# Kernel tuning notes

Hardware: AMD Instinct MI355X
Metric: run time of the kernel (lower is better)

The kernel has to match this reference:

```python
import jax, jax.numpy as jnp
import numpy as np

B, T, IN, H, OUT = 1024, 512, 16, 64, 8


def setup_inputs() -> dict:
    key = jax.random.key(0)
    ks = jax.random.split(key, 7)
    s = 1.0 / np.sqrt(H)
    return {
        "x": jax.random.normal(ks[0], (B, T, IN), dtype=jnp.float32),
        "W_ih": jax.random.normal(ks[1], (4 * H, IN), dtype=jnp.float32) * s,
        "W_hh": jax.random.normal(ks[2], (4 * H, H), dtype=jnp.float32) * s,
        "b_ih": jax.random.normal(ks[3], (4 * H,), dtype=jnp.float32) * s,
        "b_hh": jax.random.normal(ks[4], (4 * H,), dtype=jnp.float32) * s,
        "W_fc": jax.random.normal(ks[5], (OUT, H), dtype=jnp.float32) * s,
        "b_fc": jax.random.normal(ks[6], (OUT,), dtype=jnp.float32) * s,
    }


def reference(x, W_ih, W_hh, b_ih, b_hh, W_fc, b_fc):
    Bq, Tq, _ = x.shape
    Hq = W_hh.shape[1]
    # Precompute input contribution for all timesteps: [T, B, 4H]
    xw = jnp.einsum("bti,gi->tbg", x, W_ih) + b_ih + b_hh

    def step(carry, xw_t):
        h, c = carry
        gates = xw_t + h @ W_hh.T  # [B, 4H]
        i, f, g, o = jnp.split(gates, 4, axis=-1)  # PyTorch gate order i,f,g,o
        i = jax.nn.sigmoid(i)
        f = jax.nn.sigmoid(f)
        g = jnp.tanh(g)
        o = jax.nn.sigmoid(o)
        c = f * c + i * g
        h = o * jnp.tanh(c)
        return (h, c), None

    h0 = jnp.zeros((Bq, Hq), dtype=x.dtype)
    c0 = jnp.zeros((Bq, Hq), dtype=x.dtype)
    (h_last, _), _ = jax.lax.scan(step, (h0, c0), xw)

    # fc on last timestep only, then sigmoid -> [B, 1, OUT]
    out = jax.nn.sigmoid(h_last @ W_fc.T + b_fc)
    return out[:, None, :]
```

## Files before the change

kernel.cpp:

```cpp
#include <hip/hip_runtime.h>
#include <math.h>


#define LSTM_T 512
#define LSTM_IN 16
#define LSTM_H 64
#define LSTM_OUT 8
#define BT 2
#define HSTRIDE 80

#define L2E   1.44269504088896340736f
#define L2E2  2.88539008177792681472f

typedef _Float16 half8  __attribute__((ext_vector_type(8)));
typedef float    floatx4 __attribute__((ext_vector_type(4)));

static __device__ __forceinline__ float fast_rcp(float x) { return __builtin_amdgcn_rcpf(x); }
static __device__ __forceinline__ float fast_exp2(float x) { return __builtin_amdgcn_exp2f(x); }
static __device__ __forceinline__ float sigm2(float p) { return fast_rcp(1.0f + fast_exp2(-p)); }
static __device__ __forceinline__ void pin4(int4& v) {
    asm volatile("" : "+v"(v.x), "+v"(v.y), "+v"(v.z), "+v"(v.w));
}
static __device__ __forceinline__ void pinf4(float4& v) {
    asm volatile("" : "+v"(v.x), "+v"(v.y), "+v"(v.z), "+v"(v.w));
}
static __device__ __forceinline__ void lite_barrier() {
    asm volatile("s_waitcnt lgkmcnt(0)\n\ts_barrier" ::: "memory");
}
static __device__ __forceinline__ unsigned pk2h(float a, float b) {
    return __builtin_bit_cast(unsigned, __builtin_amdgcn_cvt_pkrtz(a, b));
}
static __device__ __forceinline__ half8 to_h8(float4 a, float4 b) {
    uint4 u = make_uint4(pk2h(a.x, a.y), pk2h(a.z, a.w), pk2h(b.x, b.y), pk2h(b.z, b.w));
    return __builtin_bit_cast(half8, u);
}
static __device__ __forceinline__ int4 cvt8h(float4 a, float4 b) {
    return __builtin_bit_cast(int4, to_h8(a, b));
}
static __device__ __forceinline__ float4 ld4(const float* p) {
    return *reinterpret_cast<const float4*>(p);
}
static __device__ __forceinline__ float4 scl4(float4 v, float s) {
    return make_float4(s * v.x, s * v.y, s * v.z, s * v.w);
}
static __device__ __forceinline__ float sel4(floatx4 v, bool r0, bool r1) {
    float lo = r0 ? v[1] : v[0];
    float hi = r0 ? v[3] : v[2];
    return r1 ? hi : lo;
}
static __device__ __forceinline__ float dpp8(float v) {
    int r = __builtin_amdgcn_update_dpp(0, __builtin_bit_cast(int, v),
                                        0x128, 0xF, 0xF, false);
    return __builtin_bit_cast(float, r);
}

__global__ __launch_bounds__(256, 2)
void lstm_mfma_kernel(const float* __restrict__ x,
                      const float* __restrict__ W_ih,
                      const float* __restrict__ W_hh,
                      const float* __restrict__ b_ih,
                      const float* __restrict__ b_hh,
                      const float* __restrict__ W_fc,
                      const float* __restrict__ b_fc,
                      float* __restrict__ out) {
    const int tid   = threadIdx.x;
    const int lane  = tid & 63;
    const int w     = tid >> 6;
    const int q     = lane >> 4;
    const int m     = lane & 15;
    const int b     = m & 1;
    const int rho   = (m >> 1) & 3;
    const bool r0   = (rho & 1) != 0;
    const bool r1   = (rho & 2) != 0;
    const bool h1   = (m & 8) != 0;
    const int jmine = 16 * w + 4 * q + rho;
    const int bbase = blockIdx.x * BT;

    const float a1 = h1 ? 1.0f : 0.0f;
    const float b1 = h1 ? -2.0f : 1.0f;

    __shared__ __align__(128) _Float16 hbuf[2][BT][HSTRIDE];
    __shared__ __align__(16)  float    hfin[BT][LSTM_H];

    int4 Ah[4][2], Ax[4];
    float4 bias4[4];
    #pragma unroll
    for (int tt = 0; tt < 4; ++tt) {
        const float sc = (tt == 2) ? L2E2 : -L2E;
        const int gt = tt * 64 + 16 * w + m;
        #pragma unroll
        for (int c = 0; c < 2; ++c) {
            const float* s = W_hh + gt * LSTM_H + 32 * c + 8 * q;
            Ah[tt][c] = cvt8h(scl4(ld4(s), sc), scl4(ld4(s + 4), sc));
            pin4(Ah[tt][c]);
        }
        float4 xa = make_float4(0.f, 0.f, 0.f, 0.f), xb = xa;
        if (q < 2) {
            const float* s = W_ih + gt * LSTM_IN + 8 * q;
            xa = ld4(s); xb = ld4(s + 4);
        }
        Ax[tt] = cvt8h(scl4(xa, sc), scl4(xb, sc));
        pin4(Ax[tt]);
        const int gb = tt * 64 + 16 * w + 4 * q;
        float4 bi = ld4(b_ih + gb), bh = ld4(b_hh + gb);
        bias4[tt] = make_float4(sc * (bi.x + bh.x), sc * (bi.y + bh.y),
                                sc * (bi.z + bh.z), sc * (bi.w + bh.w));
        pinf4(bias4[tt]);
    }

    if (tid < 80) {
        reinterpret_cast<int*>(&hbuf[0][0][0])[tid] = 0;
    }

    const float* xp = x + (size_t)(bbase + b) * LSTM_T * LSTM_IN + 8 * q;
    float4 xA0 = make_float4(0.f, 0.f, 0.f, 0.f), xA1 = xA0;
    float4 xB0 = xA0, xB1 = xA0;
    if (q < 2) {
        xA0 = ld4(xp);              xA1 = ld4(xp + 4);
        xB0 = ld4(xp + LSTM_IN);    xB1 = ld4(xp + LSTM_IN + 4);
    }

    floatx4 accX[4];
    {
        half8 xf = to_h8(xA0, xA1);
        #pragma unroll
        for (int tt = 0; tt < 4; ++tt)
            accX[tt] = __builtin_amdgcn_mfma_f32_16x16x32_f16(
                __builtin_bit_cast(half8, Ax[tt]), xf,
                __builtin_bit_cast(floatx4, bias4[tt]), 0, 0, 0);
    }
    if (q < 2) {
        xA0 = ld4(xp + 2 * LSTM_IN);
        xA1 = ld4(xp + 2 * LSTM_IN + 4);
    }
    __syncthreads();

    float cs = 0.0f, hreg = 0.0f;

#define STEP(T_, X0, X1)                                                        \
    {                                                                           \
        const _Float16* cur = &hbuf[(T_) & 1][0][0];                            \
        _Float16*       nxt = &hbuf[((T_) + 1) & 1][0][0];                      \
               \
        half8 bh0 = *reinterpret_cast<const half8*>(cur + b * HSTRIDE + 8 * q); \
        half8 bh1 = *reinterpret_cast<const half8*>(cur + b * HSTRIDE + 32 + 8 * q); \
                \
        floatx4 accf, accg, acci, acco;                                         \
        accf = __builtin_amdgcn_mfma_f32_16x16x32_f16(                          \
            __builtin_bit_cast(half8, Ah[1][0]), bh0, accX[1], 0, 0, 0);        \
        accg = __builtin_amdgcn_mfma_f32_16x16x32_f16(                          \
            __builtin_bit_cast(half8, Ah[2][0]), bh0, accX[2], 0, 0, 0);        \
        accf = __builtin_amdgcn_mfma_f32_16x16x32_f16(                          \
            __builtin_bit_cast(half8, Ah[1][1]), bh1, accf, 0, 0, 0);           \
        accg = __builtin_amdgcn_mfma_f32_16x16x32_f16(                          \
            __builtin_bit_cast(half8, Ah[2][1]), bh1, accg, 0, 0, 0);           \
        __builtin_amdgcn_s_setprio(1);                                          \
        float uf = sel4(accf, r0, r1);                                          \
        float ug = sel4(accg, r0, r1);                                          \
        float u1 = h1 ? ug : uf;                                                \
        float e1 = fast_exp2(u1);                                               \
        acci = __builtin_amdgcn_mfma_f32_16x16x32_f16(                          \
            __builtin_bit_cast(half8, Ah[0][0]), bh0, accX[0], 0, 0, 0);        \
        acco = __builtin_amdgcn_mfma_f32_16x16x32_f16(                          \
            __builtin_bit_cast(half8, Ah[3][0]), bh0, accX[3], 0, 0, 0);        \
        acci = __builtin_amdgcn_mfma_f32_16x16x32_f16(                          \
            __builtin_bit_cast(half8, Ah[0][1]), bh1, acci, 0, 0, 0);           \
        acco = __builtin_amdgcn_mfma_f32_16x16x32_f16(                          \
            __builtin_bit_cast(half8, Ah[3][1]), bh1, acco, 0, 0, 0);           \
        float ui = sel4(acci, r0, r1);                                          \
        float uo = sel4(acco, r0, r1);                                          \
        float u2 = h1 ? uo : ui;                                                \
        float e2 = fast_exp2(u2);                                               \
                 \
        if ((T_) + 1 < LSTM_T) {                                                \
            half8 xf = to_h8(X0, X1);                                           \
            _Pragma("unroll")                                                   \
            for (int tt = 0; tt < 4; ++tt)                                      \
                accX[tt] = __builtin_amdgcn_mfma_f32_16x16x32_f16(              \
                    __builtin_bit_cast(half8, Ax[tt]), xf,                      \
                    __builtin_bit_cast(floatx4, bias4[tt]), 0, 0, 0);           \
        }                                                                       \
                                        \
        if (q < 2 && (T_) + 3 < LSTM_T) {                                       \
            X0 = ld4(xp + (size_t)((T_) + 3) * LSTM_IN);                        \
            X1 = ld4(xp + (size_t)((T_) + 3) * LSTM_IN + 4);                    \
        }                                                                       \
        \
        float act1 = fmaf(b1, fast_rcp(1.0f + e1), a1);                         \
        float act2 = fast_rcp(1.0f + e2);                                       \
                                              \
        float g_in = dpp8(act1);                                                \
        float o_in = dpp8(act2);                                                \
                 \
        float fsel = h1 ? g_in : act1;                            \
        float isel = h1 ? o_in : act2;                            \
        float gsel = h1 ? act1 : g_in;                            \
        float osel = h1 ? act2 : o_in;                            \
        cs = fmaf(fsel, cs, (L2E2 * isel) * gsel);                              \
        float th = fmaf(-2.0f, fast_rcp(1.0f + fast_exp2(cs)), 1.0f);           \
        hreg = osel * th;                                                       \
           \
           \
        nxt[b * HSTRIDE + jmine] = (_Float16)hreg;                              \
        __builtin_amdgcn_s_setprio(0);                                          \
        lite_barrier();                                                         \
    }

    for (int t = 0; t < LSTM_T; t += 2) {
        STEP(t,     xB0, xB1)
        STEP(t + 1, xA0, xA1)
    }
#undef STEP

    hfin[b][jmine] = hreg;
    __syncthreads();

    if (tid < BT * LSTM_OUT) {
        int bb = tid >> 3, o = tid & 7;
        float s = b_fc[o];
        #pragma unroll
        for (int j4 = 0; j4 < LSTM_H / 4; ++j4) {
            float4 wv = ld4(W_fc + o * LSTM_H + 4 * j4);
            float4 hv = *reinterpret_cast<const float4*>(&hfin[bb][4 * j4]);
            s = fmaf(wv.x, hv.x, s);
            s = fmaf(wv.y, hv.y, s);
            s = fmaf(wv.z, hv.z, s);
            s = fmaf(wv.w, hv.w, s);
        }
        out[(size_t)(bbase + bb) * LSTM_OUT + o] = sigm2(s * L2E);
    }
}

extern "C" void kernel_launch(void* const* d_in, const int* in_sizes, int n_in,
                              void* d_out, int out_size, void* d_ws, size_t ws_size,
                              hipStream_t stream) {
    const float* x    = (const float*)d_in[0];
    const float* W_ih = (const float*)d_in[1];
    const float* W_hh = (const float*)d_in[2];
    const float* b_ih = (const float*)d_in[3];
    const float* b_hh = (const float*)d_in[4];
    const float* W_fc = (const float*)d_in[5];
    const float* b_fc = (const float*)d_in[6];
    float* out = (float*)d_out;

    lstm_mfma_kernel<<<1024 / BT, 256, 0, stream>>>(
        x, W_ih, W_hh, b_ih, b_hh, W_fc, b_fc, out);
}
```

Baseline: 257.1 us.

## Batch input projection for 8 timesteps into double-buffered LDS

Instead of issuing four input-projection MFMAs every timestep, each lane now computes the x·W_ih + bias contribution for one of 8 timesteps (indexed by lane bits), once per 8-step block. The results go into a double-buffered, XOR-swizzled LDS buffer. Each step reads its precomputed gate input as a float2 and adds it after the recurrent MFMAs, which now start from a zero accumulator. This removes per-step input MFMAs and global loads from the serial critical path, at the cost of extra LDS traffic, more shared memory, and scalar adds in the gate computation.

New measurement: 237.1 us. 1.08x faster.

```diff
diff --git a/kernel.cpp b/kernel.cpp
--- a/kernel.cpp
+++ b/kernel.cpp
@@ -8,6 +8,8 @@
 #define LSTM_OUT 8
 #define BT 2
 #define HSTRIDE 80
+#define XSTR 73
+#define XWSZ 2336
 
 #define L2E   1.44269504088896340736f
 #define L2E2  2.88539008177792681472f
@@ -53,6 +55,10 @@
                                         0x128, 0xF, 0xF, false);
     return __builtin_bit_cast(float, r);
 }
+
+#define MF(A_, B_, C_) __builtin_amdgcn_mfma_f32_16x16x32_f16( \
+        __builtin_bit_cast(half8, A_), (B_), (C_), 0, 0, 0)
+#define B4(i) __builtin_bit_cast(floatx4, bias4[i])
 
 __global__ __launch_bounds__(256, 2)
 void lstm_mfma_kernel(const float* __restrict__ x,
@@ -69,16 +75,19 @@
     const int q     = lane >> 4;
     const int m     = lane & 15;
     const int b     = m & 1;
+    const int dt    = m >> 1;
     const int rho   = (m >> 1) & 3;
     const bool r0   = (rho & 1) != 0;
     const bool r1   = (rho & 2) != 0;
     const bool h1   = (m & 8) != 0;
+    const int h1i   = h1 ? 1 : 0;
     const int jmine = 16 * w + 4 * q + rho;
     const int bbase = blockIdx.x * BT;
 
     const float a1 = h1 ? 1.0f : 0.0f;
     const float b1 = h1 ? -2.0f : 1.0f;
 
+    __shared__ __align__(16)  float2   xwbuf[2][XWSZ];
     __shared__ __align__(128) _Float16 hbuf[2][BT][HSTRIDE];
     __shared__ __align__(16)  float    hfin[BT][LSTM_H];
 
@@ -108,90 +117,93 @@
         pinf4(bias4[tt]);
     }
 
-    if (tid < 80) {
-        reinterpret_cast<int*>(&hbuf[0][0][0])[tid] = 0;
-    }
-
-    const float* xp = x + (size_t)(bbase + b) * LSTM_T * LSTM_IN + 8 * q;
-    float4 xA0 = make_float4(0.f, 0.f, 0.f, 0.f), xA1 = xA0;
-    float4 xB0 = xA0, xB1 = xA0;
+    float4 zc4 = make_float4(0.f, 0.f, 0.f, 0.f);
+    pinf4(zc4);
+    const floatx4 zc = __builtin_bit_cast(floatx4, zc4);
+
+    if (tid < 80) reinterpret_cast<int*>(&hbuf[0][0][0])[tid] = 0;
+
+    const float* xpb = x + (size_t)(bbase + b) * LSTM_T * LSTM_IN
+                         + (size_t)dt * LSTM_IN + 8 * q;
+    float4 Xb0 = make_float4(0.f, 0.f, 0.f, 0.f), Xb1 = Xb0;
+    if (q < 2) { Xb0 = ld4(xpb); Xb1 = ld4(xpb + 4); }
+
+    floatx4 aXi_, aXf_, aXg_, aXo_;
+    {
+        half8 xfb = to_h8(Xb0, Xb1);
+        aXi_ = MF(Ax[0], xfb, B4(0));
+        aXf_ = MF(Ax[1], xfb, B4(1));
+        aXg_ = MF(Ax[2], xfb, B4(2));
+        aXo_ = MF(Ax[3], xfb, B4(3));
+        float2* xwch = &xwbuf[0][0];
+        #pragma unroll
+        for (int r = 0; r < 4; ++r) {
+            int jw = (16 * w + 4 * q + r) ^ dt;
+            xwch[(dt * 4 + 2 * b + 0) * XSTR + jw] = make_float2(aXf_[r], aXi_[r]);
+            xwch[(dt * 4 + 2 * b + 1) * XSTR + jw] = make_float2(aXg_[r], aXo_[r]);
+        }
+    }
     if (q < 2) {
-        xA0 = ld4(xp);              xA1 = ld4(xp + 4);
-        xB0 = ld4(xp + LSTM_IN);    xB1 = ld4(xp + LSTM_IN + 4);
-    }
-
-    floatx4 accX[4];
-    {
-        half8 xf = to_h8(xA0, xA1);
-        #pragma unroll
-        for (int tt = 0; tt < 4; ++tt)
-            accX[tt] = __builtin_amdgcn_mfma_f32_16x16x32_f16(
-                __builtin_bit_cast(half8, Ax[tt]), xf,
-                __builtin_bit_cast(floatx4, bias4[tt]), 0, 0, 0);
-    }
-    if (q < 2) {
-        xA0 = ld4(xp + 2 * LSTM_IN);
-        xA1 = ld4(xp + 2 * LSTM_IN + 4);
+        Xb0 = ld4(xpb + 8 * LSTM_IN);
+        Xb1 = ld4(xpb + 8 * LSTM_IN + 4);
     }
     __syncthreads();
 
+    float2 xwc = xwbuf[0][(2 * b + h1i) * XSTR + jmine];
     float cs = 0.0f, hreg = 0.0f;
 
-#define STEP(T_, X0, X1)                                                        \
+#define STEP_CORE(T_, PK, KN, NCB, WCB, DOB)                                    \
     {                                                                           \
-        const _Float16* cur = &hbuf[(T_) & 1][0][0];                            \
-        _Float16*       nxt = &hbuf[((T_) + 1) & 1][0][0];                      \
-               \
+        const _Float16* cur = &hbuf[PK][0][0];                                  \
+        _Float16*       nxt = &hbuf[(PK) ^ 1][0][0];                            \
         half8 bh0 = *reinterpret_cast<const half8*>(cur + b * HSTRIDE + 8 * q); \
         half8 bh1 = *reinterpret_cast<const half8*>(cur + b * HSTRIDE + 32 + 8 * q); \
-                \
-        floatx4 accf, accg, acci, acco;                                         \
-        accf = __builtin_amdgcn_mfma_f32_16x16x32_f16(                          \
-            __builtin_bit_cast(half8, Ah[1][0]), bh0, accX[1], 0, 0, 0);        \
-        accg = __builtin_amdgcn_mfma_f32_16x16x32_f16(                          \
-            __builtin_bit_cast(half8, Ah[2][0]), bh0, accX[2], 0, 0, 0);        \
-        accf = __builtin_amdgcn_mfma_f32_16x16x32_f16(                          \
-            __builtin_bit_cast(half8, Ah[1][1]), bh1, accf, 0, 0, 0);           \
-        accg = __builtin_amdgcn_mfma_f32_16x16x32_f16(                          \
-            __builtin_bit_cast(half8, Ah[2][1]), bh1, accg, 0, 0, 0);           \
+        if (DOB && (T_) + 8 < LSTM_T) {       \
+            half8 xfb = to_h8(Xb0, Xb1);                                        \
+            aXi_ = MF(Ax[0], xfb, B4(0));                                       \
+            aXf_ = MF(Ax[1], xfb, B4(1));                                       \
+            aXg_ = MF(Ax[2], xfb, B4(2));                                       \
+            aXo_ = MF(Ax[3], xfb, B4(3));                                       \
+            if (q < 2 && (T_) + 16 < LSTM_T) {                                  \
+                Xb0 = ld4(xpb + (size_t)((T_) + 16) * LSTM_IN);                 \
+                Xb1 = ld4(xpb + (size_t)((T_) + 16) * LSTM_IN + 4);             \
+            }                                                                   \
+        }                                                                       \
+                 \
+        float2 xwn = xwbuf[NCB][((KN) * 4 + 2 * b + h1i) * XSTR                 \
+                                + (jmine ^ (KN))];                              \
+        floatx4 accf = MF(Ah[1][0], bh0, zc);                                   \
+        floatx4 accg = MF(Ah[2][0], bh0, zc);                                   \
+        accf = MF(Ah[1][1], bh1, accf);                                         \
+        accg = MF(Ah[2][1], bh1, accg);                                         \
         __builtin_amdgcn_s_setprio(1);                                          \
         float uf = sel4(accf, r0, r1);                                          \
         float ug = sel4(accg, r0, r1);                                          \
-        float u1 = h1 ? ug : uf;                                                \
+        float u1 = (h1 ? ug : uf) + xwc.x;                                      \
         float e1 = fast_exp2(u1);                                               \
-        acci = __builtin_amdgcn_mfma_f32_16x16x32_f16(                          \
-            __builtin_bit_cast(half8, Ah[0][0]), bh0, accX[0], 0, 0, 0);        \
-        acco = __builtin_amdgcn_mfma_f32_16x16x32_f16(                          \
-            __builtin_bit_cast(half8, Ah[3][0]), bh0, accX[3], 0, 0, 0);        \
-        acci = __builtin_amdgcn_mfma_f32_16x16x32_f16(                          \
-            __builtin_bit_cast(half8, Ah[0][1]), bh1, acci, 0, 0, 0);           \
-        acco = __builtin_amdgcn_mfma_f32_16x16x32_f16(                          \
-            __builtin_bit_cast(half8, Ah[3][1]), bh1, acco, 0, 0, 0);           \
-        float ui = sel4(acci, r0, r1);                                          \
-        float uo = sel4(acco, r0, r1);                                          \
-        float u2 = h1 ? uo : ui;                                                \
+        floatx4 acci = MF(Ah[0][0], bh0, zc);                                   \
+        floatx4 acco = MF(Ah[3][0], bh0, zc);                                   \
+        acci = MF(Ah[0][1], bh1, acci);                                         \
+        acco = MF(Ah[3][1], bh1, acco);                                         \
+        float act1 = fmaf(b1, fast_rcp(1.0f + e1), a1);                         \
+        float uii = sel4(acci, r0, r1);                                         \
+        float uoo = sel4(acco, r0, r1);                                         \
+        float u2 = (h1 ? uoo : uii) + xwc.y;                                    \
         float e2 = fast_exp2(u2);                                               \
-                 \
-        if ((T_) + 1 < LSTM_T) {                                                \
-            half8 xf = to_h8(X0, X1);                                           \
+        if (DOB && (T_) + 8 < LSTM_T) {         \
+            float2* xwch = &xwbuf[WCB][0];                                      \
             _Pragma("unroll")                                                   \
-            for (int tt = 0; tt < 4; ++tt)                                      \
-                accX[tt] = __builtin_amdgcn_mfma_f32_16x16x32_f16(              \
-                    __builtin_bit_cast(half8, Ax[tt]), xf,                      \
-                    __builtin_bit_cast(floatx4, bias4[tt]), 0, 0, 0);           \
+            for (int r = 0; r < 4; ++r) {                                       \
+                int jw = (16 * w + 4 * q + r) ^ dt;                             \
+                xwch[(dt * 4 + 2 * b + 0) * XSTR + jw] =                        \
+                    make_float2(aXf_[r], aXi_[r]);                              \
+                xwch[(dt * 4 + 2 * b + 1) * XSTR + jw] =                        \
+                    make_float2(aXg_[r], aXo_[r]);                              \
+            }                                                                   \
         }                                                                       \
-                                        \
-        if (q < 2 && (T_) + 3 < LSTM_T) {                                       \
-            X0 = ld4(xp + (size_t)((T_) + 3) * LSTM_IN);                        \
-            X1 = ld4(xp + (size_t)((T_) + 3) * LSTM_IN + 4);                    \
-        }                                                                       \
-        \
-        float act1 = fmaf(b1, fast_rcp(1.0f + e1), a1);                         \
         float act2 = fast_rcp(1.0f + e2);                                       \
-                                              \
         float g_in = dpp8(act1);                                                \
         float o_in = dpp8(act2);                                                \
-                 \
         float fsel = h1 ? g_in : act1;                            \
         float isel = h1 ? o_in : act2;                            \
         float gsel = h1 ? act1 : g_in;                            \
@@ -199,18 +211,25 @@
         cs = fmaf(fsel, cs, (L2E2 * isel) * gsel);                              \
         float th = fmaf(-2.0f, fast_rcp(1.0f + fast_exp2(cs)), 1.0f);           \
         hreg = osel * th;                                                       \
-           \
-           \
         nxt[b * HSTRIDE + jmine] = (_Float16)hreg;                              \
         __builtin_amdgcn_s_setprio(0);                                          \
         lite_barrier();                                                         \
-    }
-
-    for (int t = 0; t < LSTM_T; t += 2) {
-        STEP(t,     xB0, xB1)
-        STEP(t + 1, xA0, xA1)
-    }
-#undef STEP
+        xwc = xwn;                                                              \
+    }
+
+    for (int t8 = 0; t8 < LSTM_T; t8 += 8) {
+        const int cb = (t8 >> 3) & 1;
+        const int wb = cb ^ 1;
+        STEP_CORE(t8,     0, 1, cb, wb, 1)
+        STEP_CORE(t8 + 1, 1, 2, cb, 0, 0)
+        STEP_CORE(t8 + 2, 0, 3, cb, 0, 0)
+        STEP_CORE(t8 + 3, 1, 4, cb, 0, 0)
+        STEP_CORE(t8 + 4, 0, 5, cb, 0, 0)
+        STEP_CORE(t8 + 5, 1, 6, cb, 0, 0)
+        STEP_CORE(t8 + 6, 0, 7, cb, 0, 0)
+        STEP_CORE(t8 + 7, 1, 0, wb, 0, 0)
+    }
+#undef STEP_CORE
 
     hfin[b][jmine] = hreg;
     __syncthreads();
```
